# Performance work log

Measured on AMD Instinct MI355X. Metric: run time of the kernel, lower is better.

The kernel has to match this reference:

```python
import jax, jax.numpy as jnp
import numpy as np

K = 4
N_UP = 50
N_DOWN = 50


def setup_inputs() -> dict:
    key = jax.random.key(0)
    k1, k2, k3, k4 = jax.random.split(key, 4)
    B, N, D = 2048, 100, 128
    configs = jax.random.randint(k1, (B, N), 0, 4, dtype=jnp.int64)
    tok_table = jax.random.normal(k2, (4, D), dtype=jnp.float32)
    pos_table = jax.random.normal(k3, (144, D), dtype=jnp.float32)
    W_orb = jax.random.normal(k4, (K * (N_UP + N_DOWN), D), dtype=jnp.float32) * 0.01
    b_orb = jnp.zeros((K * (N_UP + N_DOWN),), dtype=jnp.float32)
    return {"configs": configs, "tok_table": tok_table, "pos_table": pos_table,
            "W_orb": W_orb, "b_orb": b_orb}


def _occ_idx(mask, n_occ):
    # indices of occupied sites first (stable argsort of -mask), then sorted ascending
    idx = jnp.argsort(-mask.astype(jnp.float32), axis=1)[:, :n_occ]
    return jnp.sort(idx, axis=1)


def reference(configs, tok_table, pos_table, W_orb, b_orb):
    B, N = configs.shape
    # encode_input + identity backbone
    h = tok_table[configs] + pos_table[jnp.arange(N)][None, :, :]  # (B,N,D)
    orb = jnp.einsum('bnd,od->bno', h, W_orb) + b_orb               # (B,N,K*(nu+nd))
    orb_up = orb[..., :K * N_UP].reshape(B, N, K, N_UP).transpose(0, 2, 1, 3)
    orb_dn = orb[..., K * N_UP:].reshape(B, N, K, N_DOWN).transpose(0, 2, 1, 3)
    has_up = (configs == 1) | (configs == 3)
    has_dn = (configs == 2) | (configs == 3)
    up_idx = _occ_idx(has_up, N_UP)      # (B,n_up)
    dn_idx = _occ_idx(has_dn, N_DOWN)    # (B,n_down)
    phi_up = jnp.take_along_axis(orb_up, up_idx[:, None, :, None], axis=2)  # (B,K,nu,nu)
    phi_dn = jnp.take_along_axis(orb_dn, dn_idx[:, None, :, None], axis=2)  # (B,K,nd,nd)
    det_up = jnp.linalg.det(phi_up)  # (B,K)
    det_dn = jnp.linalg.det(phi_dn)  # (B,K)
    psi = jnp.sum(det_up * det_dn, axis=1)  # (B,)
    log_abs = jnp.log(jnp.abs(psi) + 1e-30)
    phase = jnp.where(psi >= 0, 0.0, jnp.pi).astype(jnp.float32)
    return jax.lax.complex(log_abs.astype(jnp.float32), phase)
```

## Files before the change

### kernel.cpp

```cpp
#include <hip/hip_runtime.h>
#include <math.h>

#define NSITE 100
#define NOCC  50
#define DIM   128
#define KDET  4
#define NTAB  400
#define TP_FLOATS ((4 + 144) * NTAB)


__device__ __forceinline__ unsigned dpp_max64_to_lane63(unsigned x) {
  unsigned t;
  t = (unsigned)__builtin_amdgcn_update_dpp((int)x, (int)x, 0x111, 0xf, 0xf, false);
  x = x > t ? x : t;
  t = (unsigned)__builtin_amdgcn_update_dpp((int)x, (int)x, 0x112, 0xf, 0xf, false);
  x = x > t ? x : t;
  t = (unsigned)__builtin_amdgcn_update_dpp((int)x, (int)x, 0x114, 0xf, 0xf, false);
  x = x > t ? x : t;
  t = (unsigned)__builtin_amdgcn_update_dpp((int)x, (int)x, 0x118, 0xf, 0xf, false);
  x = x > t ? x : t;
  t = (unsigned)__builtin_amdgcn_update_dpp((int)x, (int)x, 0x142, 0xa, 0xf, false);
  x = x > t ? x : t;
  t = (unsigned)__builtin_amdgcn_update_dpp((int)x, (int)x, 0x143, 0xc, 0xf, false);
  x = x > t ? x : t;
  return x;
}

#define REPC(X) X(0) X(1) X(2) X(3) X(4) X(5) X(6) X(7) X(8) X(9) \
  X(10) X(11) X(12) X(13) X(14) X(15) X(16) X(17) X(18) X(19) \
  X(20) X(21) X(22) X(23) X(24)

__global__ __launch_bounds__(256) void tp_kernel(
    const float* __restrict__ tok, const float* __restrict__ pos,
    const float* __restrict__ W,   const float* __restrict__ bvec,
    float* __restrict__ T, float* __restrict__ P)
{
  const int gid = blockIdx.x * 256 + threadIdx.x;
  if (gid >= 148 * NTAB * 4) return;
  const int q   = gid >> 2;
  const int h   = gid & 3;
  const int row = q / NTAB;
  const int col = q - row * NTAB;
  const float4* h4 = (const float4*)((row < 4) ? (tok + (size_t)row * DIM)
                                               : (pos + (size_t)(row - 4) * DIM));
  const float4* w4 = (const float4*)(W + (size_t)col * DIM);
  float acc = 0.0f;
  #pragma unroll
  for (int i = 0; i < 8; ++i) {
    float4 a = h4[h * 8 + i], b = w4[h * 8 + i];
    acc = fmaf(a.x, b.x, acc);
    acc = fmaf(a.y, b.y, acc);
    acc = fmaf(a.z, b.z, acc);
    acc = fmaf(a.w, b.w, acc);
  }
  acc += __shfl_xor(acc, 1);
  acc += __shfl_xor(acc, 2);
  if (h == 0) {
    if (row < 4) T[(size_t)row * NTAB + col] = acc;
    else         P[(size_t)(row - 4) * NTAB + col] = acc + bvec[col];
  }
}

__global__ __launch_bounds__(512)
__attribute__((amdgpu_waves_per_eu(8)))
void det_kernel(
    const int*   __restrict__ configs,
    const float* __restrict__ T,
    const float* __restrict__ P,
    float*       __restrict__ out,
    int B)
{
  const int b = blockIdx.x;

  __shared__ float stash[8][25][50];
  __shared__ int cfg[NSITE];
  __shared__ int idxs[2][NOCC];
  __shared__ unsigned long long omask[2][2];
  __shared__ double detl[2][KDET][2];

  const int tid = threadIdx.x;

  int  cval = 0;
  bool ou = false, od = false;
  if (tid < NSITE) {
    cval = configs[(size_t)b * NSITE + tid];
    cfg[tid] = cval;
    ou = (cval == 1) || (cval == 3);
    od = (cval == 2) || (cval == 3);
  }
  const unsigned long long balu = __ballot(ou);
  const unsigned long long bald = __ballot(od);
  if ((tid & 63) == 0 && tid < 128) {
    omask[0][tid >> 6] = balu;
    omask[1][tid >> 6] = bald;
  }
  __syncthreads();
  if (tid < NSITE) {
    #pragma unroll
    for (int s = 0; s < 2; ++s) {
      const unsigned long long m0 = omask[s][0], m1 = omask[s][1];
      const bool occv = (s == 0) ? ou : od;
      const int mtot = __popcll(m0) + __popcll(m1);
      const int need = (mtot < NOCC) ? (NOCC - mtot) : 0;
      int pocc;
      if (tid >= 64) pocc = __popcll(m0) + __popcll(m1 & ((1ull << (tid - 64)) - 1ull));
      else           pocc = __popcll(m0 & ((1ull << tid) - 1ull));
      const int punocc = tid - pocc;
      const bool sel = occv ? (pocc < NOCC) : (punocc < need);
      const int  poscap = (pocc  < NOCC) ? pocc  : NOCC;
      const int  pfill  = (punocc < need) ? punocc : need;
      if (sel) idxs[s][poscap + pfill] = tid;
    }
  }
  __syncthreads();

  const int lane   = tid & 63;
  const int wave   = tid >> 6;
  const int wave_u = __builtin_amdgcn_readfirstlane(wave);
  const int spin   = wave_u >> 2;
  const int kd     = wave_u & 3;
  const int colbase = spin * 200 + kd * 50;

  const bool act  = (lane < NOCC);
  const int  site = idxs[spin][act ? lane : 0];
  const int  cc0  = cfg[site];
  const float* Trow = T + (size_t)cc0  * NTAB + colbase;
  const float* Prow = P + (size_t)site * NTAB + colbase;
  const float2* T2 = (const float2*)Trow;
  const float2* P2 = (const float2*)Prow;

  #define DECLC(i) float c##i;
  REPC(DECLC)
  #undef DECLC
  #define LQ(i0, i1) { float2 a = T2[(i0) / 2], d = P2[(i0) / 2]; \
      c##i0 = a.x + d.x; c##i1 = a.y + d.y; }
  LQ(0, 1)  LQ(2, 3)  LQ(4, 5)  LQ(6, 7)  LQ(8, 9)  LQ(10, 11)
  LQ(12, 13) LQ(14, 15) LQ(16, 17) LQ(18, 19) LQ(20, 21) LQ(22, 23)
  #undef LQ
  c24 = Trow[24] + Prow[24];
  #define ZC(i) c##i = act ? c##i : 0.0f;
  REPC(ZC)
  #undef ZC

  unsigned aliveq = act ? 0xFFFFFFFFu : 0u;
  float    mant_prod = 1.0f;
  int      esum = 0;
  unsigned sgnx = 0u;
  unsigned long long chosen = 0ull;
  int      invsum = 0;
  const unsigned lu = (unsigned)lane;
  unsigned long long pp[3] = {0ull, 0ull, 0ull};

  #define UC(L) { const float pc = __int_as_float( \
      __builtin_amdgcn_readlane(__float_as_int(c##L), p)); \
      c##L = fmaf(-mult, pc, c##L); }
  #define UCF_25
  #define UCF_24 UC(24)
  #define UCF_23 UC(23) UCF_24
  #define UCF_22 UC(22) UCF_23
  #define UCF_21 UC(21) UCF_22
  #define UCF_20 UC(20) UCF_21
  #define UCF_19 UC(19) UCF_20
  #define UCF_18 UC(18) UCF_19
  #define UCF_17 UC(17) UCF_18
  #define UCF_16 UC(16) UCF_17
  #define UCF_15 UC(15) UCF_16
  #define UCF_14 UC(14) UCF_15
  #define UCF_13 UC(13) UCF_14
  #define UCF_12 UC(12) UCF_13
  #define UCF_11 UC(11) UCF_12
  #define UCF_10 UC(10) UCF_11
  #define UCF_9  UC(9)  UCF_10
  #define UCF_8  UC(8)  UCF_9
  #define UCF_7  UC(7)  UCF_8
  #define UCF_6  UC(6)  UCF_7
  #define UCF_5  UC(5)  UCF_6
  #define UCF_4  UC(4)  UCF_5
  #define UCF_3  UC(3)  UCF_4
  #define UCF_2  UC(2)  UCF_3
  #define UCF_1  UC(1)  UCF_2

  #define P1STEP(J, N) { \
    unsigned key = ((__float_as_uint(c##J) & 0x7FFFFFC0u) | lu) & aliveq; \
    key = dpp_max64_to_lane63(key); \
    const int p = __builtin_amdgcn_readlane((int)key, 63) & 63; \
    const unsigned pb = (unsigned)__builtin_amdgcn_readlane( \
        __float_as_int(c##J), p); \
    esum += (int)((pb >> 23) & 0xFFu) - 127; \
    sgnx ^= (pb & 0x80000000u); \
    mant_prod *= __uint_as_float((pb & 0x007FFFFFu) | 0x3F800000u); \
    invsum += __popcll(chosen >> (p + 1)); \
    chosen |= 1ull << (unsigned)p; \
    aliveq = (lane == p) ? 0u : aliveq; \
    pp[(J) / 10] |= ((unsigned long long)(unsigned)p) << (6 * ((J) % 10)); \
    const float piv = __uint_as_float(pb); \
    float r0 = __builtin_amdgcn_rcpf(piv); \
    r0 = fmaf(fmaf(-piv, r0, 1.0f), r0, r0); \
    const float rp = ((pb & 0x7FFFFFFFu) != 0u) ? r0 : 0.0f; \
    const float mult = __uint_as_float(__float_as_uint(c##J * rp) & aliveq); \
    if (act) stash[wave_u][(J)][lane] = mult; \
    UCF_##N \
  }

  P1STEP(0,1)   P1STEP(1,2)   P1STEP(2,3)   P1STEP(3,4)   P1STEP(4,5)
  P1STEP(5,6)   P1STEP(6,7)   P1STEP(7,8)   P1STEP(8,9)   P1STEP(9,10)
  P1STEP(10,11) P1STEP(11,12) P1STEP(12,13) P1STEP(13,14) P1STEP(14,15)
  P1STEP(15,16) P1STEP(16,17) P1STEP(17,18) P1STEP(18,19) P1STEP(19,20)
  P1STEP(20,21) P1STEP(21,22) P1STEP(22,23) P1STEP(23,24) P1STEP(24,25)
  #undef P1STEP

  #define DECLT(i) float t##i;
  REPC(DECLT)
  #undef DECLT
  #define LT(i) t##i = Trow[25 + (i)] + Prow[25 + (i)];
  REPC(LT)
  #undef LT
  #define ZT(i) t##i = act ? t##i : 0.0f;
  REPC(ZT)
  #undef ZT

  #define BT(L) { const float pc = __int_as_float( \
      __builtin_amdgcn_ds_bpermute(pa, __float_as_int(t##L))); \
      t##L = fmaf(-mult, pc, t##L); }

  #define P2J(J) { \
    const int pa = ((int)((pp[(J) / 10] >> (6 * ((J) % 10))) & 63ull)) << 2; \
    const float mult = stash[wave_u][(J)][lane < NOCC ? lane : 0]; \
    BT(0)  BT(1)  BT(2)  BT(3)  BT(4)  BT(5) \
    __builtin_amdgcn_sched_barrier(0); \
    BT(6)  BT(7)  BT(8)  BT(9)  BT(10) BT(11) \
    __builtin_amdgcn_sched_barrier(0); \
    BT(12) BT(13) BT(14) BT(15) BT(16) BT(17) \
    __builtin_amdgcn_sched_barrier(0); \
    BT(18) BT(19) BT(20) BT(21) BT(22) BT(23) BT(24) \
    __builtin_amdgcn_sched_barrier(0); \
  }
  P2J(0)  P2J(1)  P2J(2)  P2J(3)  P2J(4)  P2J(5)  P2J(6)  P2J(7)
  P2J(8)  P2J(9)  P2J(10) P2J(11) P2J(12) P2J(13) P2J(14) P2J(15)
  P2J(16) P2J(17) P2J(18) P2J(19) P2J(20) P2J(21) P2J(22) P2J(23)
  P2J(24)
  #undef P2J
  #undef BT

  #define UT(L) { const float pc = __int_as_float( \
      __builtin_amdgcn_readlane(__float_as_int(t##L), p)); \
      t##L = fmaf(-mult, pc, t##L); }
  #define UTF_25
  #define UTF_24 UT(24)
  #define UTF_23 UT(23) UTF_24
  #define UTF_22 UT(22) UTF_23
  #define UTF_21 UT(21) UTF_22
  #define UTF_20 UT(20) UTF_21
  #define UTF_19 UT(19) UTF_20
  #define UTF_18 UT(18) UTF_19
  #define UTF_17 UT(17) UTF_18
  #define UTF_16 UT(16) UTF_17
  #define UTF_15 UT(15) UTF_16
  #define UTF_14 UT(14) UTF_15
  #define UTF_13 UT(13) UTF_14
  #define UTF_12 UT(12) UTF_13
  #define UTF_11 UT(11) UTF_12
  #define UTF_10 UT(10) UTF_11
  #define UTF_9  UT(9)  UTF_10
  #define UTF_8  UT(8)  UTF_9
  #define UTF_7  UT(7)  UTF_8
  #define UTF_6  UT(6)  UTF_7
  #define UTF_5  UT(5)  UTF_6
  #define UTF_4  UT(4)  UTF_5
  #define UTF_3  UT(3)  UTF_4
  #define UTF_2  UT(2)  UTF_3
  #define UTF_1  UT(1)  UTF_2

  #define P3STEP(L, N) { \
    unsigned key = ((__float_as_uint(t##L) & 0x7FFFFFC0u) | lu) & aliveq; \
    key = dpp_max64_to_lane63(key); \
    const int p = __builtin_amdgcn_readlane((int)key, 63) & 63; \
    const unsigned pb = (unsigned)__builtin_amdgcn_readlane( \
        __float_as_int(t##L), p); \
    esum += (int)((pb >> 23) & 0xFFu) - 127; \
    sgnx ^= (pb & 0x80000000u); \
    mant_prod *= __uint_as_float((pb & 0x007FFFFFu) | 0x3F800000u); \
    invsum += __popcll(chosen >> (p + 1)); \
    chosen |= 1ull << (unsigned)p; \
    aliveq = (lane == p) ? 0u : aliveq; \
    const float piv = __uint_as_float(pb); \
    float r0 = __builtin_amdgcn_rcpf(piv); \
    r0 = fmaf(fmaf(-piv, r0, 1.0f), r0, r0); \
    const float rp = ((pb & 0x7FFFFFFFu) != 0u) ? r0 : 0.0f; \
    const float mult = __uint_as_float(__float_as_uint(t##L * rp) & aliveq); \
    UTF_##N \
  }

  P3STEP(0,1)   P3STEP(1,2)   P3STEP(2,3)   P3STEP(3,4)   P3STEP(4,5)
  P3STEP(5,6)   P3STEP(6,7)   P3STEP(7,8)   P3STEP(8,9)   P3STEP(9,10)
  P3STEP(10,11) P3STEP(11,12) P3STEP(12,13) P3STEP(13,14) P3STEP(14,15)
  P3STEP(15,16) P3STEP(16,17) P3STEP(17,18) P3STEP(18,19) P3STEP(19,20)
  P3STEP(20,21) P3STEP(21,22) P3STEP(22,23) P3STEP(23,24) P3STEP(24,25)
  #undef P3STEP
  #undef UT
  #undef UC

  const double logdet =
      log((double)mant_prod) + (double)esum * 0.6931471805599453;
  const int sgn = (((sgnx >> 31) + (unsigned)invsum) & 1u) ? -1 : 1;

  if (lane == 0) {
    detl[spin][kd][0] = logdet;
    detl[spin][kd][1] = (double)sgn;
  }
  __syncthreads();

  if (tid == 0) {
    double t[KDET], s[KDET], m = -1e300;
    #pragma unroll
    for (int k2 = 0; k2 < KDET; ++k2) {
      t[k2] = detl[0][k2][0] + detl[1][k2][0];
      s[k2] = detl[0][k2][1] * detl[1][k2][1];
      if (t[k2] > m) m = t[k2];
    }
    double sum = 0.0;
    #pragma unroll
    for (int k2 = 0; k2 < KDET; ++k2) {
      if (t[k2] > -1e290) sum += s[k2] * exp(t[k2] - m);
    }
    double pw = (m > -1e290) ? exp(m) * fabs(sum) : 0.0;
    double la = log(pw + 1e-30);
    out[b]     = (float)la;
    out[B + b] = (sum >= 0.0) ? 0.0f : 3.14159265358979f;
  }
}

extern "C" void kernel_launch(void* const* d_in, const int* in_sizes, int n_in,
                              void* d_out, int out_size, void* d_ws, size_t ws_size,
                              hipStream_t stream) {
  const int*   configs = (const int*)  d_in[0];
  const float* tok     = (const float*)d_in[1];
  const float* pos     = (const float*)d_in[2];
  const float* W       = (const float*)d_in[3];
  const float* bv      = (const float*)d_in[4];

  float*  wsf  = (float*)d_ws;
  float*  T    = wsf;
  float*  P    = wsf + 4 * NTAB;
  const int B = in_sizes[0] / NSITE;

  tp_kernel<<<(148 * NTAB * 4 + 255) / 256, 256, 0, stream>>>(tok, pos, W, bv, T, P);
  det_kernel<<<B, 512, 0, stream>>>(configs, T, P, (float*)d_out, B);
}
```

Baseline: 195.2 us.

## Block LU panel updates in groups of five columns with deferred bpermute trailing updates

Phases 1 and 3 of the wave-level LU determinant used to update every remaining column with readlane broadcasts after each pivot step. They now work in blocked panels of five columns. Pivots inside a panel still update only the panel's columns through readlane, and the trailing columns receive deferred rank-5 updates through ds_bpermute, grouped with scheduling barriers. The aim is to cut the serial chain of scalar readlane updates and let the LDS-permute traffic overlap. The cost is more register pressure from keeping five multipliers and pivot addresses live at once.

Result: slower. 272.8 us (+39.8%).

```diff
diff --git a/kernel.cpp b/kernel.cpp
--- a/kernel.cpp
+++ b/kernel.cpp
@@ -6,7 +6,6 @@
 #define DIM   128
 #define KDET  4
 #define NTAB  400
-#define TP_FLOATS ((4 + 144) * NTAB)
 
 
 __device__ __forceinline__ unsigned dpp_max64_to_lane63(unsigned x) {
@@ -151,63 +150,164 @@
   const unsigned lu = (unsigned)lane;
   unsigned long long pp[3] = {0ull, 0ull, 0ull};
 
-  #define UC(L) { const float pc = __int_as_float( \
-      __builtin_amdgcn_readlane(__float_as_int(c##L), p)); \
-      c##L = fmaf(-mult, pc, c##L); }
-  #define UCF_25
-  #define UCF_24 UC(24)
-  #define UCF_23 UC(23) UCF_24
-  #define UCF_22 UC(22) UCF_23
-  #define UCF_21 UC(21) UCF_22
-  #define UCF_20 UC(20) UCF_21
-  #define UCF_19 UC(19) UCF_20
-  #define UCF_18 UC(18) UCF_19
-  #define UCF_17 UC(17) UCF_18
-  #define UCF_16 UC(16) UCF_17
-  #define UCF_15 UC(15) UCF_16
-  #define UCF_14 UC(14) UCF_15
-  #define UCF_13 UC(13) UCF_14
-  #define UCF_12 UC(12) UCF_13
-  #define UCF_11 UC(11) UCF_12
-  #define UCF_10 UC(10) UCF_11
-  #define UCF_9  UC(9)  UCF_10
-  #define UCF_8  UC(8)  UCF_9
-  #define UCF_7  UC(7)  UCF_8
-  #define UCF_6  UC(6)  UCF_7
-  #define UCF_5  UC(5)  UCF_6
-  #define UCF_4  UC(4)  UCF_5
-  #define UCF_3  UC(3)  UCF_4
-  #define UCF_2  UC(2)  UCF_3
-  #define UCF_1  UC(1)  UCF_2
-
-  #define P1STEP(J, N) { \
-    unsigned key = ((__float_as_uint(c##J) & 0x7FFFFFC0u) | lu) & aliveq; \
+  #define PSTEP(JIDX, CJ, MV, PV) { \
+    unsigned key = ((__float_as_uint(CJ) & 0x7FFFFFC0u) | lu) & aliveq; \
     key = dpp_max64_to_lane63(key); \
-    const int p = __builtin_amdgcn_readlane((int)key, 63) & 63; \
+    PV = __builtin_amdgcn_readlane((int)key, 63) & 63; \
     const unsigned pb = (unsigned)__builtin_amdgcn_readlane( \
-        __float_as_int(c##J), p); \
+        __float_as_int(CJ), PV); \
     esum += (int)((pb >> 23) & 0xFFu) - 127; \
     sgnx ^= (pb & 0x80000000u); \
     mant_prod *= __uint_as_float((pb & 0x007FFFFFu) | 0x3F800000u); \
-    invsum += __popcll(chosen >> (p + 1)); \
-    chosen |= 1ull << (unsigned)p; \
-    aliveq = (lane == p) ? 0u : aliveq; \
-    pp[(J) / 10] |= ((unsigned long long)(unsigned)p) << (6 * ((J) % 10)); \
+    invsum += __popcll(chosen >> (PV + 1)); \
+    chosen |= 1ull << (unsigned)PV; \
+    aliveq = (lane == PV) ? 0u : aliveq; \
+    pp[(JIDX) / 10] |= ((unsigned long long)(unsigned)PV) << (6 * ((JIDX) % 10)); \
     const float piv = __uint_as_float(pb); \
     float r0 = __builtin_amdgcn_rcpf(piv); \
     r0 = fmaf(fmaf(-piv, r0, 1.0f), r0, r0); \
     const float rp = ((pb & 0x7FFFFFFFu) != 0u) ? r0 : 0.0f; \
-    const float mult = __uint_as_float(__float_as_uint(c##J * rp) & aliveq); \
-    if (act) stash[wave_u][(J)][lane] = mult; \
-    UCF_##N \
-  }
-
-  P1STEP(0,1)   P1STEP(1,2)   P1STEP(2,3)   P1STEP(3,4)   P1STEP(4,5)
-  P1STEP(5,6)   P1STEP(6,7)   P1STEP(7,8)   P1STEP(8,9)   P1STEP(9,10)
-  P1STEP(10,11) P1STEP(11,12) P1STEP(12,13) P1STEP(13,14) P1STEP(14,15)
-  P1STEP(15,16) P1STEP(16,17) P1STEP(17,18) P1STEP(18,19) P1STEP(19,20)
-  P1STEP(20,21) P1STEP(21,22) P1STEP(22,23) P1STEP(23,24) P1STEP(24,25)
-  #undef P1STEP
+    MV = __uint_as_float(__float_as_uint((CJ) * rp) & aliveq); \
+    if (act) stash[wave_u][(JIDX)][lane] = MV; }
+
+  #define PSTEP3(CJ, MV, PV) { \
+    unsigned key = ((__float_as_uint(CJ) & 0x7FFFFFC0u) | lu) & aliveq; \
+    key = dpp_max64_to_lane63(key); \
+    PV = __builtin_amdgcn_readlane((int)key, 63) & 63; \
+    const unsigned pb = (unsigned)__builtin_amdgcn_readlane( \
+        __float_as_int(CJ), PV); \
+    esum += (int)((pb >> 23) & 0xFFu) - 127; \
+    sgnx ^= (pb & 0x80000000u); \
+    mant_prod *= __uint_as_float((pb & 0x007FFFFFu) | 0x3F800000u); \
+    invsum += __popcll(chosen >> (PV + 1)); \
+    chosen |= 1ull << (unsigned)PV; \
+    aliveq = (lane == PV) ? 0u : aliveq; \
+    const float piv = __uint_as_float(pb); \
+    float r0 = __builtin_amdgcn_rcpf(piv); \
+    r0 = fmaf(fmaf(-piv, r0, 1.0f), r0, r0); \
+    const float rp = ((pb & 0x7FFFFFFFu) != 0u) ? r0 : 0.0f; \
+    MV = __uint_as_float(__float_as_uint((CJ) * rp) & aliveq); }
+
+  #define RLU(CL, MV, PV) { const float pc = __int_as_float( \
+      __builtin_amdgcn_readlane(__float_as_int(CL), PV)); \
+      CL = fmaf(-(MV), pc, CL); }
+  #define BPU(CL, MV, AV) { const float pc = __int_as_float( \
+      __builtin_amdgcn_ds_bpermute(AV, __float_as_int(CL))); \
+      CL = fmaf(-(MV), pc, CL); }
+  #define BP5(Ca,Cb,Cc,Cd,Ce,M,A) \
+      BPU(Ca,M,A) BPU(Cb,M,A) BPU(Cc,M,A) BPU(Cd,M,A) BPU(Ce,M,A)
+
+  {
+    float m0,m1,m2,m3,m4; int q0_,q1_,q2_,q3_,q4_;
+    PSTEP(0, c0, m0, q0_)
+    RLU(c1,m0,q0_) RLU(c2,m0,q0_) RLU(c3,m0,q0_) RLU(c4,m0,q0_)
+    PSTEP(1, c1, m1, q1_)
+    RLU(c2,m1,q1_) RLU(c3,m1,q1_) RLU(c4,m1,q1_)
+    PSTEP(2, c2, m2, q2_)
+    RLU(c3,m2,q2_) RLU(c4,m2,q2_)
+    PSTEP(3, c3, m3, q3_)
+    RLU(c4,m3,q3_)
+    PSTEP(4, c4, m4, q4_)
+    const int a0=q0_<<2,a1=q1_<<2,a2=q2_<<2,a3=q3_<<2,a4=q4_<<2;
+    BP5(c5,c6,c7,c8,c9,m0,a0) BP5(c10,c11,c12,c13,c14,m0,a0)
+    BP5(c15,c16,c17,c18,c19,m0,a0) BP5(c20,c21,c22,c23,c24,m0,a0)
+    __builtin_amdgcn_sched_barrier(0);
+    BP5(c5,c6,c7,c8,c9,m1,a1) BP5(c10,c11,c12,c13,c14,m1,a1)
+    BP5(c15,c16,c17,c18,c19,m1,a1) BP5(c20,c21,c22,c23,c24,m1,a1)
+    __builtin_amdgcn_sched_barrier(0);
+    BP5(c5,c6,c7,c8,c9,m2,a2) BP5(c10,c11,c12,c13,c14,m2,a2)
+    BP5(c15,c16,c17,c18,c19,m2,a2) BP5(c20,c21,c22,c23,c24,m2,a2)
+    __builtin_amdgcn_sched_barrier(0);
+    BP5(c5,c6,c7,c8,c9,m3,a3) BP5(c10,c11,c12,c13,c14,m3,a3)
+    BP5(c15,c16,c17,c18,c19,m3,a3) BP5(c20,c21,c22,c23,c24,m3,a3)
+    __builtin_amdgcn_sched_barrier(0);
+    BP5(c5,c6,c7,c8,c9,m4,a4) BP5(c10,c11,c12,c13,c14,m4,a4)
+    BP5(c15,c16,c17,c18,c19,m4,a4) BP5(c20,c21,c22,c23,c24,m4,a4)
+    __builtin_amdgcn_sched_barrier(0);
+  }
+  {
+    float m0,m1,m2,m3,m4; int q0_,q1_,q2_,q3_,q4_;
+    PSTEP(5, c5, m0, q0_)
+    RLU(c6,m0,q0_) RLU(c7,m0,q0_) RLU(c8,m0,q0_) RLU(c9,m0,q0_)
+    PSTEP(6, c6, m1, q1_)
+    RLU(c7,m1,q1_) RLU(c8,m1,q1_) RLU(c9,m1,q1_)
+    PSTEP(7, c7, m2, q2_)
+    RLU(c8,m2,q2_) RLU(c9,m2,q2_)
+    PSTEP(8, c8, m3, q3_)
+    RLU(c9,m3,q3_)
+    PSTEP(9, c9, m4, q4_)
+    const int a0=q0_<<2,a1=q1_<<2,a2=q2_<<2,a3=q3_<<2,a4=q4_<<2;
+    BP5(c10,c11,c12,c13,c14,m0,a0) BP5(c15,c16,c17,c18,c19,m0,a0)
+    BP5(c20,c21,c22,c23,c24,m0,a0)
+    __builtin_amdgcn_sched_barrier(0);
+    BP5(c10,c11,c12,c13,c14,m1,a1) BP5(c15,c16,c17,c18,c19,m1,a1)
+    BP5(c20,c21,c22,c23,c24,m1,a1)
+    __builtin_amdgcn_sched_barrier(0);
+    BP5(c10,c11,c12,c13,c14,m2,a2) BP5(c15,c16,c17,c18,c19,m2,a2)
+    BP5(c20,c21,c22,c23,c24,m2,a2)
+    __builtin_amdgcn_sched_barrier(0);
+    BP5(c10,c11,c12,c13,c14,m3,a3) BP5(c15,c16,c17,c18,c19,m3,a3)
+    BP5(c20,c21,c22,c23,c24,m3,a3)
+    __builtin_amdgcn_sched_barrier(0);
+    BP5(c10,c11,c12,c13,c14,m4,a4) BP5(c15,c16,c17,c18,c19,m4,a4)
+    BP5(c20,c21,c22,c23,c24,m4,a4)
+    __builtin_amdgcn_sched_barrier(0);
+  }
+  {
+    float m0,m1,m2,m3,m4; int q0_,q1_,q2_,q3_,q4_;
+    PSTEP(10, c10, m0, q0_)
+    RLU(c11,m0,q0_) RLU(c12,m0,q0_) RLU(c13,m0,q0_) RLU(c14,m0,q0_)
+    PSTEP(11, c11, m1, q1_)
+    RLU(c12,m1,q1_) RLU(c13,m1,q1_) RLU(c14,m1,q1_)
+    PSTEP(12, c12, m2, q2_)
+    RLU(c13,m2,q2_) RLU(c14,m2,q2_)
+    PSTEP(13, c13, m3, q3_)
+    RLU(c14,m3,q3_)
+    PSTEP(14, c14, m4, q4_)
+    const int a0=q0_<<2,a1=q1_<<2,a2=q2_<<2,a3=q3_<<2,a4=q4_<<2;
+    BP5(c15,c16,c17,c18,c19,m0,a0) BP5(c20,c21,c22,c23,c24,m0,a0)
+    __builtin_amdgcn_sched_barrier(0);
+    BP5(c15,c16,c17,c18,c19,m1,a1) BP5(c20,c21,c22,c23,c24,m1,a1)
+    __builtin_amdgcn_sched_barrier(0);
+    BP5(c15,c16,c17,c18,c19,m2,a2) BP5(c20,c21,c22,c23,c24,m2,a2)
+    __builtin_amdgcn_sched_barrier(0);
+    BP5(c15,c16,c17,c18,c19,m3,a3) BP5(c20,c21,c22,c23,c24,m3,a3)
+    __builtin_amdgcn_sched_barrier(0);
+    BP5(c15,c16,c17,c18,c19,m4,a4) BP5(c20,c21,c22,c23,c24,m4,a4)
+    __builtin_amdgcn_sched_barrier(0);
+  }
+  {
+    float m0,m1,m2,m3,m4; int q0_,q1_,q2_,q3_,q4_;
+    PSTEP(15, c15, m0, q0_)
+    RLU(c16,m0,q0_) RLU(c17,m0,q0_) RLU(c18,m0,q0_) RLU(c19,m0,q0_)
+    PSTEP(16, c16, m1, q1_)
+    RLU(c17,m1,q1_) RLU(c18,m1,q1_) RLU(c19,m1,q1_)
+    PSTEP(17, c17, m2, q2_)
+    RLU(c18,m2,q2_) RLU(c19,m2,q2_)
+    PSTEP(18, c18, m3, q3_)
+    RLU(c19,m3,q3_)
+    PSTEP(19, c19, m4, q4_)
+    const int a0=q0_<<2,a1=q1_<<2,a2=q2_<<2,a3=q3_<<2,a4=q4_<<2;
+    BP5(c20,c21,c22,c23,c24,m0,a0)
+    BP5(c20,c21,c22,c23,c24,m1,a1)
+    BP5(c20,c21,c22,c23,c24,m2,a2)
+    BP5(c20,c21,c22,c23,c24,m3,a3)
+    BP5(c20,c21,c22,c23,c24,m4,a4)
+    __builtin_amdgcn_sched_barrier(0);
+  }
+  {
+    float m0,m1,m2,m3,m4; int q0_,q1_,q2_,q3_,q4_;
+    PSTEP(20, c20, m0, q0_)
+    RLU(c21,m0,q0_) RLU(c22,m0,q0_) RLU(c23,m0,q0_) RLU(c24,m0,q0_)
+    PSTEP(21, c21, m1, q1_)
+    RLU(c22,m1,q1_) RLU(c23,m1,q1_) RLU(c24,m1,q1_)
+    PSTEP(22, c22, m2, q2_)
+    RLU(c23,m2,q2_) RLU(c24,m2,q2_)
+    PSTEP(23, c23, m3, q3_)
+    RLU(c24,m3,q3_)
+    PSTEP(24, c24, m4, q4_)
+    (void)m0;(void)m1;(void)m2;(void)m3;(void)m4;
+  }
 
   #define DECLT(i) float t##i;
   REPC(DECLT)
@@ -242,63 +342,117 @@
   #undef P2J
   #undef BT
 
-  #define UT(L) { const float pc = __int_as_float( \
-      __builtin_amdgcn_readlane(__float_as_int(t##L), p)); \
-      t##L = fmaf(-mult, pc, t##L); }
-  #define UTF_25
-  #define UTF_24 UT(24)
-  #define UTF_23 UT(23) UTF_24
-  #define UTF_22 UT(22) UTF_23
-  #define UTF_21 UT(21) UTF_22
-  #define UTF_20 UT(20) UTF_21
-  #define UTF_19 UT(19) UTF_20
-  #define UTF_18 UT(18) UTF_19
-  #define UTF_17 UT(17) UTF_18
-  #define UTF_16 UT(16) UTF_17
-  #define UTF_15 UT(15) UTF_16
-  #define UTF_14 UT(14) UTF_15
-  #define UTF_13 UT(13) UTF_14
-  #define UTF_12 UT(12) UTF_13
-  #define UTF_11 UT(11) UTF_12
-  #define UTF_10 UT(10) UTF_11
-  #define UTF_9  UT(9)  UTF_10
-  #define UTF_8  UT(8)  UTF_9
-  #define UTF_7  UT(7)  UTF_8
-  #define UTF_6  UT(6)  UTF_7
-  #define UTF_5  UT(5)  UTF_6
-  #define UTF_4  UT(4)  UTF_5
-  #define UTF_3  UT(3)  UTF_4
-  #define UTF_2  UT(2)  UTF_3
-  #define UTF_1  UT(1)  UTF_2
-
-  #define P3STEP(L, N) { \
-    unsigned key = ((__float_as_uint(t##L) & 0x7FFFFFC0u) | lu) & aliveq; \
-    key = dpp_max64_to_lane63(key); \
-    const int p = __builtin_amdgcn_readlane((int)key, 63) & 63; \
-    const unsigned pb = (unsigned)__builtin_amdgcn_readlane( \
-        __float_as_int(t##L), p); \
-    esum += (int)((pb >> 23) & 0xFFu) - 127; \
-    sgnx ^= (pb & 0x80000000u); \
-    mant_prod *= __uint_as_float((pb & 0x007FFFFFu) | 0x3F800000u); \
-    invsum += __popcll(chosen >> (p + 1)); \
-    chosen |= 1ull << (unsigned)p; \
-    aliveq = (lane == p) ? 0u : aliveq; \
-    const float piv = __uint_as_float(pb); \
-    float r0 = __builtin_amdgcn_rcpf(piv); \
-    r0 = fmaf(fmaf(-piv, r0, 1.0f), r0, r0); \
-    const float rp = ((pb & 0x7FFFFFFFu) != 0u) ? r0 : 0.0f; \
-    const float mult = __uint_as_float(__float_as_uint(t##L * rp) & aliveq); \
-    UTF_##N \
-  }
-
-  P3STEP(0,1)   P3STEP(1,2)   P3STEP(2,3)   P3STEP(3,4)   P3STEP(4,5)
-  P3STEP(5,6)   P3STEP(6,7)   P3STEP(7,8)   P3STEP(8,9)   P3STEP(9,10)
-  P3STEP(10,11) P3STEP(11,12) P3STEP(12,13) P3STEP(13,14) P3STEP(14,15)
-  P3STEP(15,16) P3STEP(16,17) P3STEP(17,18) P3STEP(18,19) P3STEP(19,20)
-  P3STEP(20,21) P3STEP(21,22) P3STEP(22,23) P3STEP(23,24) P3STEP(24,25)
-  #undef P3STEP
-  #undef UT
-  #undef UC
+  {
+    float m0,m1,m2,m3,m4; int q0_,q1_,q2_,q3_,q4_;
+    PSTEP3(t0, m0, q0_)
+    RLU(t1,m0,q0_) RLU(t2,m0,q0_) RLU(t3,m0,q0_) RLU(t4,m0,q0_)
+    PSTEP3(t1, m1, q1_)
+    RLU(t2,m1,q1_) RLU(t3,m1,q1_) RLU(t4,m1,q1_)
+    PSTEP3(t2, m2, q2_)
+    RLU(t3,m2,q2_) RLU(t4,m2,q2_)
+    PSTEP3(t3, m3, q3_)
+    RLU(t4,m3,q3_)
+    PSTEP3(t4, m4, q4_)
+    const int a0=q0_<<2,a1=q1_<<2,a2=q2_<<2,a3=q3_<<2,a4=q4_<<2;
+    BP5(t5,t6,t7,t8,t9,m0,a0) BP5(t10,t11,t12,t13,t14,m0,a0)
+    BP5(t15,t16,t17,t18,t19,m0,a0) BP5(t20,t21,t22,t23,t24,m0,a0)
+    __builtin_amdgcn_sched_barrier(0);
+    BP5(t5,t6,t7,t8,t9,m1,a1) BP5(t10,t11,t12,t13,t14,m1,a1)
+    BP5(t15,t16,t17,t18,t19,m1,a1) BP5(t20,t21,t22,t23,t24,m1,a1)
+    __builtin_amdgcn_sched_barrier(0);
+    BP5(t5,t6,t7,t8,t9,m2,a2) BP5(t10,t11,t12,t13,t14,m2,a2)
+    BP5(t15,t16,t17,t18,t19,m2,a2) BP5(t20,t21,t22,t23,t24,m2,a2)
+    __builtin_amdgcn_sched_barrier(0);
+    BP5(t5,t6,t7,t8,t9,m3,a3) BP5(t10,t11,t12,t13,t14,m3,a3)
+    BP5(t15,t16,t17,t18,t19,m3,a3) BP5(t20,t21,t22,t23,t24,m3,a3)
+    __builtin_amdgcn_sched_barrier(0);
+    BP5(t5,t6,t7,t8,t9,m4,a4) BP5(t10,t11,t12,t13,t14,m4,a4)
+    BP5(t15,t16,t17,t18,t19,m4,a4) BP5(t20,t21,t22,t23,t24,m4,a4)
+    __builtin_amdgcn_sched_barrier(0);
+  }
+  {
+    float m0,m1,m2,m3,m4; int q0_,q1_,q2_,q3_,q4_;
+    PSTEP3(t5, m0, q0_)
+    RLU(t6,m0,q0_) RLU(t7,m0,q0_) RLU(t8,m0,q0_) RLU(t9,m0,q0_)
+    PSTEP3(t6, m1, q1_)
+    RLU(t7,m1,q1_) RLU(t8,m1,q1_) RLU(t9,m1,q1_)
+    PSTEP3(t7, m2, q2_)
+    RLU(t8,m2,q2_) RLU(t9,m2,q2_)
+    PSTEP3(t8, m3, q3_)
+    RLU(t9,m3,q3_)
+    PSTEP3(t9, m4, q4_)
+    const int a0=q0_<<2,a1=q1_<<2,a2=q2_<<2,a3=q3_<<2,a4=q4_<<2;
+    BP5(t10,t11,t12,t13,t14,m0,a0) BP5(t15,t16,t17,t18,t19,m0,a0)
+    BP5(t20,t21,t22,t23,t24,m0,a0)
+    __builtin_amdgcn_sched_barrier(0);
+    BP5(t10,t11,t12,t13,t14,m1,a1) BP5(t15,t16,t17,t18,t19,m1,a1)
+    BP5(t20,t21,t22,t23,t24,m1,a1)
+    __builtin_amdgcn_sched_barrier(0);
+    BP5(t10,t11,t12,t13,t14,m2,a2) BP5(t15,t16,t17,t18,t19,m2,a2)
+    BP5(t20,t21,t22,t23,t24,m2,a2)
+    __builtin_amdgcn_sched_barrier(0);
+    BP5(t10,t11,t12,t13,t14,m3,a3) BP5(t15,t16,t17,t18,t19,m3,a3)
+    BP5(t20,t21,t22,t23,t24,m3,a3)
+    __builtin_amdgcn_sched_barrier(0);
+    BP5(t10,t11,t12,t13,t14,m4,a4) BP5(t15,t16,t17,t18,t19,m4,a4)
+    BP5(t20,t21,t22,t23,t24,m4,a4)
+    __builtin_amdgcn_sched_barrier(0);
+  }
+  {
+    float m0,m1,m2,m3,m4; int q0_,q1_,q2_,q3_,q4_;
+    PSTEP3(t10, m0, q0_)
+    RLU(t11,m0,q0_) RLU(t12,m0,q0_) RLU(t13,m0,q0_) RLU(t14,m0,q0_)
+    PSTEP3(t11, m1, q1_)
+    RLU(t12,m1,q1_) RLU(t13,m1,q1_) RLU(t14,m1,q1_)
+    PSTEP3(t12, m2, q2_)
+    RLU(t13,m2,q2_) RLU(t14,m2,q2_)
+    PSTEP3(t13, m3, q3_)
+    RLU(t14,m3,q3_)
+    PSTEP3(t14, m4, q4_)
+    const int a0=q0_<<2,a1=q1_<<2,a2=q2_<<2,a3=q3_<<2,a4=q4_<<2;
+    BP5(t15,t16,t17,t18,t19,m0,a0) BP5(t20,t21,t22,t23,t24,m0,a0)
+    __builtin_amdgcn_sched_barrier(0);
+    BP5(t15,t16,t17,t18,t19,m1,a1) BP5(t20,t21,t22,t23,t24,m1,a1)
+    __builtin_amdgcn_sched_barrier(0);
+    BP5(t15,t16,t17,t18,t19,m2,a2) BP5(t20,t21,t22,t23,t24,m2,a2)
+    __builtin_amdgcn_sched_barrier(0);
+    BP5(t15,t16,t17,t18,t19,m3,a3) BP5(t20,t21,t22,t23,t24,m3,a3)
+    __builtin_amdgcn_sched_barrier(0);
+    BP5(t15,t16,t17,t18,t19,m4,a4) BP5(t20,t21,t22,t23,t24,m4,a4)
+    __builtin_amdgcn_sched_barrier(0);
+  }
+  {
+    float m0,m1,m2,m3,m4; int q0_,q1_,q2_,q3_,q4_;
+    PSTEP3(t15, m0, q0_)
+    RLU(t16,m0,q0_) RLU(t17,m0,q0_) RLU(t18,m0,q0_) RLU(t19,m0,q0_)
+    PSTEP3(t16, m1, q1_)
+    RLU(t17,m1,q1_) RLU(t18,m1,q1_) RLU(t19,m1,q1_)
+    PSTEP3(t17, m2, q2_)
+    RLU(t18,m2,q2_) RLU(t19,m2,q2_)
+    PSTEP3(t18, m3, q3_)
+    RLU(t19,m3,q3_)
+    PSTEP3(t19, m4, q4_)
+    const int a0=q0_<<2,a1=q1_<<2,a2=q2_<<2,a3=q3_<<2,a4=q4_<<2;
+    BP5(t20,t21,t22,t23,t24,m0,a0)
+    BP5(t20,t21,t22,t23,t24,m1,a1)
+    BP5(t20,t21,t22,t23,t24,m2,a2)
+    BP5(t20,t21,t22,t23,t24,m3,a3)
+    BP5(t20,t21,t22,t23,t24,m4,a4)
+    __builtin_amdgcn_sched_barrier(0);
+  }
+  {
+    float m0,m1,m2,m3,m4; int q0_,q1_,q2_,q3_,q4_;
+    PSTEP3(t20, m0, q0_)
+    RLU(t21,m0,q0_) RLU(t22,m0,q0_) RLU(t23,m0,q0_) RLU(t24,m0,q0_)
+    PSTEP3(t21, m1, q1_)
+    RLU(t22,m1,q1_) RLU(t23,m1,q1_) RLU(t24,m1,q1_)
+    PSTEP3(t22, m2, q2_)
+    RLU(t23,m2,q2_) RLU(t24,m2,q2_)
+    PSTEP3(t23, m3, q3_)
+    RLU(t24,m3,q3_)
+    PSTEP3(t24, m4, q4_)
+    (void)m0;(void)m1;(void)m2;(void)m3;(void)m4;
+  }
 
   const double logdet =
       log((double)mant_prod) + (double)esum * 0.6931471805599453;
```
